# Performance work log

Hardware: AMD Instinct MI355X
Metric: run time of the kernel (lower is better)

## Reference

```python
import jax, jax.numpy as jnp
import numpy as np


def setup_inputs() -> dict:
    key = jax.random.key(0)
    k1, k2 = jax.random.split(key)
    B, C, H, W = 8, 19, 512, 512
    pred = jax.random.normal(k1, (B, C, H, W), dtype=jnp.float32)
    target = jax.random.randint(k2, (B, H, W), 0, C)
    return {"pred": pred, "target": target}


def reference(pred, target):
    B, C, H, W = pred.shape
    N = H * W
    p = jax.nn.softmax(pred, axis=1).reshape(B, C, N)                      # [B,C,N]
    # one-hot float target per class: target_flat = (target == c).float()
    tgt = (target.reshape(B, 1, N) == jnp.arange(C)[None, :, None]).astype(p.dtype)  # [B,C,N]
    signs = 2.0 * tgt - 1.0
    errors = 1.0 - p * signs                                               # [B,C,N]
    # descending sort of errors; permutation applied to the target too
    perm = jnp.argsort(-errors, axis=-1)                                   # [B,C,N]
    errors_sorted = jnp.take_along_axis(errors, perm, axis=-1)
    gt_sorted = jnp.take_along_axis(tgt, perm, axis=-1)
    # Lovasz gradient (Jaccard extension gradient)
    gts = jnp.sum(gt_sorted, axis=-1, keepdims=True)                       # [B,C,1]
    intersection = gts - jnp.cumsum(gt_sorted, axis=-1)
    union = gts + jnp.cumsum(1.0 - gt_sorted, axis=-1)
    jaccard = 1.0 - intersection / union
    grad = jnp.concatenate([jaccard[..., :1], jaccard[..., 1:] - jaccard[..., :-1]], axis=-1)
    # dot(relu(errors_sorted), grad) per (b,c), then mean over B*C
    loss_bc = jnp.sum(jax.nn.relu(errors_sorted) * grad, axis=-1)          # [B,C]
    return jnp.sum(loss_bc) / (B * C)
```

## Files before the change

kernel.cpp:

```cpp
#include <hip/hip_runtime.h>

#define BATCH 8
#define NCLS  19
#define LOGN  18
#define NPIX  (1u << LOGN)
#define NB    64
#define BLK1  512
#define BPB   64
#define PPB   (NPIX / BPB)
#define HCOPY 8
#define HSTR  (NCLS * NB + 4)

struct Buf {
    float2 x[NCLS];
    int2   tg;
};

__device__ __forceinline__ void load_buf(Buf& bf, const float* __restrict__ pb,
                                         const int* __restrict__ tb, int n) {
    bf.tg = *reinterpret_cast<const int2*>(tb + n);
    #pragma unroll
    for (int c = 0; c < NCLS; ++c)
        bf.x[c] = *reinterpret_cast<const float2*>(pb + ((size_t)c << LOGN) + n);
}

__device__ __forceinline__ void process(const Buf& bf, unsigned* __restrict__ hpar,
                                        float* __restrict__ s2lds,
                                        unsigned* __restrict__ cntlds) {
    float2 e2[NCLS];
    float sA = 0.f, sB = 0.f;
    #pragma unroll
    for (int c = 0; c < NCLS; ++c) {
        const float eA = __expf(bf.x[c].x);
        const float eB = __expf(bf.x[c].y);
        e2[c].x = eA; e2[c].y = eB;
        sA += eA; sB += eB;
    }
    const float rA = __builtin_amdgcn_rcpf(sA) * (float)NB;
    const float rB = __builtin_amdgcn_rcpf(sB) * (float)NB;
    const int tgA = bf.tg.x, tgB = bf.tg.y;
    float etA = 0.f, etB = 0.f;
    #pragma unroll
    for (int c = 0; c < NCLS; ++c) {
        const float tA = e2[c].x * rA;
        const float tB = e2[c].y * rB;
        etA = (c == tgA) ? e2[c].x : etA;
        etB = (c == tgB) ? e2[c].y : etB;
        int binA = (int)tA; binA = binA > NB - 1 ? NB - 1 : binA;
        int binB = (int)tB; binB = binB > NB - 1 ? NB - 1 : binB;
        if (c != tgA && binA != 0) atomicAdd(&hpar[c * NB + binA], 1u);
        if (c != tgB && binB != 0) atomicAdd(&hpar[c * NB + binB], 1u);
    }
    const float s2A = fmaf(etA * rA, -1.0f / (float)NB, 1.0f);
    const float s2B = fmaf(etB * rB, -1.0f / (float)NB, 1.0f);
    atomicAdd(&s2lds[tgA], s2A);
    atomicAdd(&s2lds[tgB], s2B);
    atomicAdd(&cntlds[tgA], 1u);
    atomicAdd(&cntlds[tgB], 1u);
}

__global__ __launch_bounds__(BLK1, 4) void k_hist(
    const float* __restrict__ pred, const int* __restrict__ target,
    unsigned short* __restrict__ hist_part, float* __restrict__ s2_part,
    unsigned short* __restrict__ cnt_part)
{
    __shared__ unsigned hist[HCOPY * HSTR];
    __shared__ float    s2lds[NCLS];
    __shared__ unsigned cntlds[NCLS];

    const int b     = blockIdx.x / BPB;
    const int chunk = blockIdx.x % BPB;
    const int tid   = threadIdx.x;
    const int lane  = tid & 63;

    unsigned* hpar = hist + (lane & (HCOPY - 1)) * HSTR;

    for (int i = tid; i < HCOPY * HSTR; i += BLK1) hist[i] = 0u;
    if (tid < NCLS) { s2lds[tid] = 0.f; cntlds[tid] = 0u; }
    __syncthreads();

    const float* pb = pred + (((size_t)b * NCLS) << LOGN);
    const int*   tb = target + ((size_t)b << LOGN);
    const int    base = chunk * PPB + 2 * tid;

    Buf A, B;
    load_buf(A, pb, tb, base);
    load_buf(B, pb, tb, base + 2 * BLK1);
    process(A, hpar, s2lds, cntlds);
    load_buf(A, pb, tb, base + 4 * BLK1);
    process(B, hpar, s2lds, cntlds);
    load_buf(B, pb, tb, base + 6 * BLK1);
    process(A, hpar, s2lds, cntlds);
    process(B, hpar, s2lds, cntlds);

    __syncthreads();

    for (int i = tid; i < NCLS * NB; i += BLK1) {
        unsigned v = 0;
        #pragma unroll
        for (int k = 0; k < HCOPY; ++k) v += hist[k * HSTR + i];
        const int c = i >> 6, bin = i & (NB - 1);
        hist_part[((size_t)(b * NCLS + c) * BPB + chunk) * NB + bin] = (unsigned short)v;
    }
    if (tid < NCLS) {
        s2_part [(size_t)(b * NCLS + tid) * BPB + chunk] = s2lds[tid];
        cnt_part[(size_t)(b * NCLS + tid) * BPB + chunk] = (unsigned short)cntlds[tid];
    }
}

__global__ __launch_bounds__(256) void k_finish(
    const unsigned short* __restrict__ hist_part, const float* __restrict__ s2_part,
    const unsigned short* __restrict__ cnt_part, float* __restrict__ loss_bc)
{
    __shared__ unsigned hsum[4][NB];
    __shared__ float s2tot, nctot;

    const int bc   = blockIdx.x;
    const int tid  = threadIdx.x;
    const int lane = tid & 63;
    const int w    = tid >> 6;

    const unsigned short* hp = hist_part + (size_t)bc * BPB * NB;
    unsigned h = 0;
    #pragma unroll 1
    for (int k = 0; k < BPB / 4; ++k)
        h += hp[(size_t)(w * (BPB / 4) + k) * NB + lane];
    hsum[w][lane] = h;

    if (w == 1) {
        float v = s2_part[(size_t)bc * BPB + lane];
        #pragma unroll
        for (int off = 32; off > 0; off >>= 1) v += __shfl_down(v, off, 64);
        if (lane == 0) s2tot = v;
    }
    if (w == 2) {
        unsigned v = cnt_part[(size_t)bc * BPB + lane];
        #pragma unroll
        for (int off = 32; off > 0; off >>= 1) v += __shfl_down(v, off, 64);
        if (lane == 0) nctot = (float)v;
    }
    __syncthreads();

    if (w == 0) {
        const unsigned hb = hsum[0][lane] + hsum[1][lane] + hsum[2][lane] + hsum[3][lane];
        const unsigned hrev = __shfl(hb, 63 - lane, 64);
        unsigned sc = hrev;
        #pragma unroll
        for (int off = 1; off < 64; off <<= 1) {
            const unsigned v = __shfl_up(sc, off, 64);
            if (lane >= off) sc += v;
        }
        const float ncf = nctot;
        const float Nf  = (float)NPIX;
        const float Mf  = Nf - ncf;
        const unsigned Rab = sc - hrev;
        float fRh = (float)sc;
        if (lane == 63) fRh = Mf;
        const float gR  = (Rab > 0)   ? (float)Rab / ((float)Rab + ncf) : 0.0f;
        const float gRh = (fRh > 0.f) ? fRh / (fRh + ncf) : 0.0f;
        float red = gR + gRh;
        #pragma unroll
        for (int off = 32; off > 0; off >>= 1) red += __shfl_down(red, off, 64);
        if (lane == 0)
            loss_bc[bc] = Mf / Nf + red * (0.5f / (float)NB) + s2tot / Nf;
    }
}

__global__ __launch_bounds__(256) void k_reduce(
    const float* __restrict__ loss_bc, float* __restrict__ out)
{
    __shared__ float r[256];
    const int tid = threadIdx.x;
    r[tid] = (tid < BATCH * NCLS) ? loss_bc[tid] : 0.0f;
    __syncthreads();
    for (int off = 128; off > 0; off >>= 1) {
        if (tid < off) r[tid] += r[tid + off];
        __syncthreads();
    }
    if (tid == 0) out[0] = r[0] * (1.0f / (float)(BATCH * NCLS));
}

extern "C" void kernel_launch(void* const* d_in, const int* in_sizes, int n_in,
                              void* d_out, int out_size, void* d_ws, size_t ws_size,
                              hipStream_t stream)
{
    const float* pred   = (const float*)d_in[0];
    const int*   target = (const int*)d_in[1];
    float*       out    = (float*)d_out;
    unsigned char* ws   = (unsigned char*)d_ws;

    unsigned short* hist_part = (unsigned short*)ws;
    size_t off = (size_t)BATCH * NCLS * BPB * NB * sizeof(unsigned short);
    float* s2_part = (float*)(ws + off);
    off += (size_t)BATCH * NCLS * BPB * sizeof(float);
    unsigned short* cnt_part = (unsigned short*)(ws + off);
    off += (size_t)BATCH * NCLS * BPB * sizeof(unsigned short);
    float* loss_bc = (float*)(ws + off);

    hipLaunchKernelGGL(k_hist,   dim3(BATCH * BPB),  dim3(BLK1), 0, stream,
                       pred, target, hist_part, s2_part, cnt_part);
    hipLaunchKernelGGL(k_finish, dim3(BATCH * NCLS), dim3(256),  0, stream,
                       hist_part, s2_part, cnt_part, loss_bc);
    hipLaunchKernelGGL(k_reduce, dim3(1),            dim3(256),  0, stream,
                       loss_bc, out);
}
```

Measured before the change: 45.73 us.

## Double block count per batch and simplify per-thread loop to one pixel

Templates the kernels on blocks-per-batch and picks 128 blocks per batch when the workspace is large enough, halving pixels per block. The histogram kernel drops the manual double-buffered float2 loads and instead loops over one pixel per thread per iteration with scalar loads, and raises the launch-bounds occupancy hint to 8. The finish kernel now loops over more partials. This trades explicit load pipelining and vector loads for more blocks and occupancy, at the cost of more partial histograms to write and reduce.

```diff
diff --git a/kernel.cpp b/kernel.cpp
--- a/kernel.cpp
+++ b/kernel.cpp
@@ -6,64 +6,18 @@
 #define NPIX  (1u << LOGN)
 #define NB    64
 #define BLK1  512
-#define BPB   64
-#define PPB   (NPIX / BPB)
 #define HCOPY 8
 #define HSTR  (NCLS * NB + 4)
 
-struct Buf {
-    float2 x[NCLS];
-    int2   tg;
-};
-
-__device__ __forceinline__ void load_buf(Buf& bf, const float* __restrict__ pb,
-                                         const int* __restrict__ tb, int n) {
-    bf.tg = *reinterpret_cast<const int2*>(tb + n);
-    #pragma unroll
-    for (int c = 0; c < NCLS; ++c)
-        bf.x[c] = *reinterpret_cast<const float2*>(pb + ((size_t)c << LOGN) + n);
-}
-
-__device__ __forceinline__ void process(const Buf& bf, unsigned* __restrict__ hpar,
-                                        float* __restrict__ s2lds,
-                                        unsigned* __restrict__ cntlds) {
-    float2 e2[NCLS];
-    float sA = 0.f, sB = 0.f;
-    #pragma unroll
-    for (int c = 0; c < NCLS; ++c) {
-        const float eA = __expf(bf.x[c].x);
-        const float eB = __expf(bf.x[c].y);
-        e2[c].x = eA; e2[c].y = eB;
-        sA += eA; sB += eB;
-    }
-    const float rA = __builtin_amdgcn_rcpf(sA) * (float)NB;
-    const float rB = __builtin_amdgcn_rcpf(sB) * (float)NB;
-    const int tgA = bf.tg.x, tgB = bf.tg.y;
-    float etA = 0.f, etB = 0.f;
-    #pragma unroll
-    for (int c = 0; c < NCLS; ++c) {
-        const float tA = e2[c].x * rA;
-        const float tB = e2[c].y * rB;
-        etA = (c == tgA) ? e2[c].x : etA;
-        etB = (c == tgB) ? e2[c].y : etB;
-        int binA = (int)tA; binA = binA > NB - 1 ? NB - 1 : binA;
-        int binB = (int)tB; binB = binB > NB - 1 ? NB - 1 : binB;
-        if (c != tgA && binA != 0) atomicAdd(&hpar[c * NB + binA], 1u);
-        if (c != tgB && binB != 0) atomicAdd(&hpar[c * NB + binB], 1u);
-    }
-    const float s2A = fmaf(etA * rA, -1.0f / (float)NB, 1.0f);
-    const float s2B = fmaf(etB * rB, -1.0f / (float)NB, 1.0f);
-    atomicAdd(&s2lds[tgA], s2A);
-    atomicAdd(&s2lds[tgB], s2B);
-    atomicAdd(&cntlds[tgA], 1u);
-    atomicAdd(&cntlds[tgB], 1u);
-}
-
-__global__ __launch_bounds__(BLK1, 4) void k_hist(
+template<int BPB>
+__global__ __launch_bounds__(BLK1, 8) void k_hist(
     const float* __restrict__ pred, const int* __restrict__ target,
     unsigned short* __restrict__ hist_part, float* __restrict__ s2_part,
     unsigned short* __restrict__ cnt_part)
 {
+    constexpr int PPB = (int)(NPIX / BPB);
+    constexpr int PXT = PPB / BLK1;
+
     __shared__ unsigned hist[HCOPY * HSTR];
     __shared__ float    s2lds[NCLS];
     __shared__ unsigned cntlds[NCLS];
@@ -81,18 +35,32 @@
 
     const float* pb = pred + (((size_t)b * NCLS) << LOGN);
     const int*   tb = target + ((size_t)b << LOGN);
-    const int    base = chunk * PPB + 2 * tid;
 
-    Buf A, B;
-    load_buf(A, pb, tb, base);
-    load_buf(B, pb, tb, base + 2 * BLK1);
-    process(A, hpar, s2lds, cntlds);
-    load_buf(A, pb, tb, base + 4 * BLK1);
-    process(B, hpar, s2lds, cntlds);
-    load_buf(B, pb, tb, base + 6 * BLK1);
-    process(A, hpar, s2lds, cntlds);
-    process(B, hpar, s2lds, cntlds);
+    #pragma unroll 1
+    for (int it = 0; it < PXT; ++it) {
+        const int n  = chunk * PPB + it * BLK1 + tid;
+        const int tg = tb[n];
 
+        float e[NCLS];
+        float s = 0.f;
+        #pragma unroll
+        for (int c = 0; c < NCLS; ++c) {
+            e[c] = __expf(pb[((size_t)c << LOGN) + n]);
+            s += e[c];
+        }
+        const float r = __builtin_amdgcn_rcpf(s) * (float)NB;
+
+        float et = 0.f;
+        #pragma unroll
+        for (int c = 0; c < NCLS; ++c) {
+            const float t = e[c] * r;
+            int bin = (int)t; bin = bin > NB - 1 ? NB - 1 : bin;
+            et = (c == tg) ? e[c] : et;
+            if (c != tg && bin != 0) atomicAdd(&hpar[c * NB + bin], 1u);
+        }
+        atomicAdd(&s2lds[tg], fmaf(et * r, -1.0f / (float)NB, 1.0f));
+        atomicAdd(&cntlds[tg], 1u);
+    }
     __syncthreads();
 
     for (int i = tid; i < NCLS * NB; i += BLK1) {
@@ -108,6 +76,7 @@
     }
 }
 
+template<int BPB>
 __global__ __launch_bounds__(256) void k_finish(
     const unsigned short* __restrict__ hist_part, const float* __restrict__ s2_part,
     const unsigned short* __restrict__ cnt_part, float* __restrict__ loss_bc)
@@ -128,13 +97,15 @@
     hsum[w][lane] = h;
 
     if (w == 1) {
-        float v = s2_part[(size_t)bc * BPB + lane];
+        float v = 0.f;
+        for (int k = lane; k < BPB; k += 64) v += s2_part[(size_t)bc * BPB + k];
         #pragma unroll
         for (int off = 32; off > 0; off >>= 1) v += __shfl_down(v, off, 64);
         if (lane == 0) s2tot = v;
     }
     if (w == 2) {
-        unsigned v = cnt_part[(size_t)bc * BPB + lane];
+        unsigned v = 0;
+        for (int k = lane; k < BPB; k += 64) v += cnt_part[(size_t)bc * BPB + k];
         #pragma unroll
         for (int off = 32; off > 0; off >>= 1) v += __shfl_down(v, off, 64);
         if (lane == 0) nctot = (float)v;
@@ -180,6 +151,26 @@
     if (tid == 0) out[0] = r[0] * (1.0f / (float)(BATCH * NCLS));
 }
 
+template<int BPB>
+static void launch_all(const float* pred, const int* target, unsigned char* ws,
+                       float* out, hipStream_t stream)
+{
+    unsigned short* hist_part = (unsigned short*)ws;
+    size_t off = (size_t)BATCH * NCLS * BPB * NB * sizeof(unsigned short);
+    float* s2_part = (float*)(ws + off);
+    off += (size_t)BATCH * NCLS * BPB * sizeof(float);
+    unsigned short* cnt_part = (unsigned short*)(ws + off);
+    off += (size_t)BATCH * NCLS * BPB * sizeof(unsigned short);
+    float* loss_bc = (float*)(ws + off);
+
+    hipLaunchKernelGGL(k_hist<BPB>,   dim3(BATCH * BPB),  dim3(BLK1), 0, stream,
+                       pred, target, hist_part, s2_part, cnt_part);
+    hipLaunchKernelGGL(k_finish<BPB>, dim3(BATCH * NCLS), dim3(256),  0, stream,
+                       hist_part, s2_part, cnt_part, loss_bc);
+    hipLaunchKernelGGL(k_reduce,      dim3(1),            dim3(256),  0, stream,
+                       loss_bc, out);
+}
+
 extern "C" void kernel_launch(void* const* d_in, const int* in_sizes, int n_in,
                               void* d_out, int out_size, void* d_ws, size_t ws_size,
                               hipStream_t stream)
@@ -189,18 +180,12 @@
     float*       out    = (float*)d_out;
     unsigned char* ws   = (unsigned char*)d_ws;
 
-    unsigned short* hist_part = (unsigned short*)ws;
-    size_t off = (size_t)BATCH * NCLS * BPB * NB * sizeof(unsigned short);
-    float* s2_part = (float*)(ws + off);
-    off += (size_t)BATCH * NCLS * BPB * sizeof(float);
-    unsigned short* cnt_part = (unsigned short*)(ws + off);
-    off += (size_t)BATCH * NCLS * BPB * sizeof(unsigned short);
-    float* loss_bc = (float*)(ws + off);
+    auto need = [](int bpb) {
+        return (size_t)BATCH * NCLS * bpb * (NB * sizeof(unsigned short)
+                                             + sizeof(float) + sizeof(unsigned short))
+             + (size_t)BATCH * NCLS * sizeof(float);
+    };
 
-    hipLaunchKernelGGL(k_hist,   dim3(BATCH * BPB),  dim3(BLK1), 0, stream,
-                       pred, target, hist_part, s2_part, cnt_part);
-    hipLaunchKernelGGL(k_finish, dim3(BATCH * NCLS), dim3(256),  0, stream,
-                       hist_part, s2_part, cnt_part, loss_bc);
-    hipLaunchKernelGGL(k_reduce, dim3(1),            dim3(256),  0, stream,
-                       loss_bc, out);
+    if (ws_size >= need(128))     launch_all<128>(pred, target, ws, out, stream);
+    else                          launch_all<64>(pred, target, ws, out, stream);
 }
```

Result: faster. 44.77 us (-2.1%).
